# Performance work log

Hardware: AMD Instinct MI355X
Metric: run time of the kernel (lower is better)

## Reference

```python
import jax, jax.numpy as jnp
import numpy as np

T = 5          # Newton-Schulz iterations
EPS = 1e-05


def reference(X):
    # X: (B, C, L); training-mode IterNorm whitening with num_groups=1
    B, C, L = X.shape
    x = jnp.transpose(X, (1, 0, 2)).reshape(C, -1)        # (d, m)
    d, m = x.shape
    mean = jnp.mean(x, axis=-1, keepdims=True)
    xc = x - mean                                         # (d, m)
    I = jnp.eye(d, dtype=X.dtype)
    Sigma = I * EPS + (xc @ xc.T) * (1.0 / m)             # (d, d)
    rTr = 1.0 / jnp.trace(Sigma)                          # scalar
    Sigma_N = Sigma * rTr
    P = I
    for _ in range(T):
        P = 1.5 * P - 0.5 * (P @ P @ P) @ Sigma_N
    wm = P * jnp.sqrt(rTr)                                # whitening matrix
    xn = wm @ xc                                          # (d, m)
    Xn = jnp.transpose(xn.reshape(C, B, L), (1, 0, 2))
    return Xn


def setup_inputs() -> dict:
    key = jax.random.key(0)
    X = jax.random.normal(key, (32, 64, 8192), dtype=jnp.float32)
    return {"X": X}
```

## Files before the change

kernel.cpp:

```cpp
#include <hip/hip_runtime.h>
#include <math.h>

#define L_DIM   8192
#define NCH     64
#define M_TOT_F 262144.0f
#define EPS_F   1e-5f

typedef float f32x4 __attribute__((ext_vector_type(4)));
typedef short bf16x8 __attribute__((ext_vector_type(8)));

union U8 { unsigned u[4]; bf16x8 v; };

__device__ __forceinline__ void cvt2(float f0, float f1, unsigned& h, unsigned& l) {
    unsigned u0 = __float_as_uint(f0), u1 = __float_as_uint(f1);
    h = (u0 >> 16) | (u1 & 0xFFFF0000u);
    float r0 = f0 - __uint_as_float(u0 & 0xFFFF0000u);
    float r1 = f1 - __uint_as_float(u1 & 0xFFFF0000u);
    l = (__float_as_uint(r0) >> 16) | (__float_as_uint(r1) & 0xFFFF0000u);
}

__device__ __forceinline__ void cvt8(const float* p, bf16x8& hi, bf16x8& lo) {
    float4 f0 = *(const float4*)p;
    float4 f1 = *(const float4*)(p + 4);
    U8 H, L;
    cvt2(f0.x, f0.y, H.u[0], L.u[0]);
    cvt2(f0.z, f0.w, H.u[1], L.u[1]);
    cvt2(f1.x, f1.y, H.u[2], L.u[2]);
    cvt2(f1.z, f1.w, H.u[3], L.u[3]);
    hi = H.v; lo = L.v;
}

__device__ __forceinline__ f32x4 mfma16(bf16x8 a, bf16x8 b, f32x4 c) {
    return __builtin_amdgcn_mfma_f32_16x16x32_bf16(a, b, c, 0, 0, 0);
}

__device__ __forceinline__ f32x4 fzero() {
    f32x4 z; z[0] = 0.f; z[1] = 0.f; z[2] = 0.f; z[3] = 0.f; return z;
}

#define GTPB 8
__global__ __launch_bounds__(256) void gram_kernel(const float* __restrict__ X,
                                                   float* __restrict__ P) {
    __shared__ __align__(16) unsigned short hplane[64 * 72];
    __shared__ __align__(16) unsigned short lplane[64 * 72];
    const int tid  = threadIdx.x;
    const int w    = tid >> 6;
    const int lane = tid & 63;
    const int m    = lane & 15;
    const int q    = lane >> 4;
    const int lrow = tid >> 2;
    const int lq16 = (tid & 3) << 4;

    f32x4 acc1[4], acc2[4];
#pragma unroll
    for (int nb = 0; nb < 4; ++nb) { acc1[nb] = fzero(); acc2[nb] = fzero(); }
    float sacc = 0.f;

    const int tile0 = blockIdx.x * GTPB;
    float4 v[4];
    {
        int t = tile0;
        const float* src = X + ((size_t)((t >> 7) * NCH + lrow)) * L_DIM + ((t & 127) << 6) + lq16;
#pragma unroll
        for (int i = 0; i < 4; ++i) v[i] = ((const float4*)src)[i];
    }

    for (int t = 0; t < GTPB; ++t) {
#pragma unroll
        for (int i = 0; i < 4; ++i) sacc += v[i].x + v[i].y + v[i].z + v[i].w;
        __syncthreads();
#pragma unroll
        for (int i = 0; i < 4; ++i) {
            unsigned h0, l0, h1, l1;
            cvt2(v[i].x, v[i].y, h0, l0);
            cvt2(v[i].z, v[i].w, h1, l1);
            uint2 hh; hh.x = h0; hh.y = h1;
            uint2 ll; ll.x = l0; ll.y = l1;
            *(uint2*)&hplane[lrow * 72 + lq16 + 4 * i] = hh;
            *(uint2*)&lplane[lrow * 72 + lq16 + 4 * i] = ll;
        }
        __syncthreads();
        if (t + 1 < GTPB) {
            int tn = tile0 + t + 1;
            const float* src = X + ((size_t)((tn >> 7) * NCH + lrow)) * L_DIM + ((tn & 127) << 6) + lq16;
#pragma unroll
            for (int i = 0; i < 4; ++i) v[i] = ((const float4*)src)[i];
        }
#pragma unroll
        for (int k0 = 0; k0 < 64; k0 += 32) {
            bf16x8 a = *(const bf16x8*)&hplane[(16 * w + m) * 72 + k0 + 8 * q];
#pragma unroll
            for (int nb = 0; nb < 4; ++nb) {
                bf16x8 bh = *(const bf16x8*)&hplane[(16 * nb + m) * 72 + k0 + 8 * q];
                bf16x8 bl = *(const bf16x8*)&lplane[(16 * nb + m) * 72 + k0 + 8 * q];
                acc1[nb] = mfma16(a, bh, acc1[nb]);
                acc2[nb] = mfma16(a, bl, acc2[nb]);
            }
        }
    }

    float* base = P + (size_t)blockIdx.x * 8256;
#pragma unroll
    for (int nb = 0; nb < 4; ++nb)
#pragma unroll
        for (int r = 0; r < 4; ++r) {
            int grow = 16 * w + 4 * q + r;
            int gcol = 16 * nb + m;
            base[grow * 64 + gcol]        = acc1[nb][r];
            base[4096 + grow * 64 + gcol] = acc2[nb][r];
        }
    sacc += __shfl_xor(sacc, 1);
    sacc += __shfl_xor(sacc, 2);
    if ((tid & 3) == 0) base[8192 + lrow] = sacc;
}

__global__ __launch_bounds__(256) void reduce_kernel(const float* __restrict__ P,
                                                     float* __restrict__ ws) {
    const int tid = threadIdx.x;
    const int w = tid >> 6, lane = tid & 63;
    const int e0 = blockIdx.x * 64;
    float a = 0.f;
#pragma unroll 8
    for (int i = 0; i < 128; ++i)
        a += P[(size_t)(w * 128 + i) * 8256 + e0 + lane];
    __shared__ float red[4][64];
    red[w][lane] = a;
    __syncthreads();
    if (w == 0)
        ws[e0 + lane] = red[0][lane] + red[1][lane] + red[2][lane] + red[3][lane];
}

__device__ __forceinline__ void mm_sym(float* __restrict__ D, const float* __restrict__ A,
                                       const float* __restrict__ B, int w, int m, int q) {
    f32x4 acc[4];
#pragma unroll
    for (int nb = 0; nb < 4; ++nb) acc[nb] = fzero();
#pragma unroll
    for (int k0 = 0; k0 < 64; k0 += 32) {
        bf16x8 ah, al;
        cvt8(&A[(16 * w + m) * 68 + k0 + 8 * q], ah, al);
#pragma unroll
        for (int nb = 0; nb < 4; ++nb) {
            bf16x8 bh, bl;
            cvt8(&B[(16 * nb + m) * 68 + k0 + 8 * q], bh, bl);
            acc[nb] = mfma16(ah, bh, acc[nb]);
            acc[nb] = mfma16(ah, bl, acc[nb]);
            acc[nb] = mfma16(al, bh, acc[nb]);
        }
    }
#pragma unroll
    for (int nb = 0; nb < 4; ++nb)
#pragma unroll
        for (int r = 0; r < 4; ++r)
            D[(16 * w + 4 * q + r) * 68 + 16 * nb + m] = acc[nb][r];
}

__global__ __launch_bounds__(256) void ns_kernel(float* __restrict__ ws) {
    __shared__ __align__(16) float S[64 * 68];
    __shared__ __align__(16) float Pm[64 * 68];
    __shared__ __align__(16) float T1[64 * 68];
    __shared__ __align__(16) float T2[64 * 68];
    __shared__ float mu[64];
    __shared__ float scal[2];

    const int tid = threadIdx.x;
    const int w = tid >> 6, lane = tid & 63;
    const int m = lane & 15, q = lane >> 4;
    const float inv_m = 1.0f / M_TOT_F;

    if (tid < 64) mu[tid] = ws[8192 + tid] * inv_m;
    __syncthreads();

    for (int e = tid; e < 4096; e += 256) {
        int i = e >> 6, j = e & 63;
        float g = (ws[e] + ws[4096 + e] + ws[4096 + (j << 6) + i]) * inv_m;
        S[i * 68 + j]  = g - mu[i] * mu[j] + ((i == j) ? EPS_F : 0.f);
        Pm[i * 68 + j] = (i == j) ? 1.f : 0.f;
    }
    __syncthreads();

    if (tid < 64) {
        float v = S[tid * 68 + tid];
#pragma unroll
        for (int off = 32; off >= 1; off >>= 1) v += __shfl_xor(v, off);
        if (tid == 0) { scal[0] = 1.0f / v; scal[1] = sqrtf(1.0f / v); }
    }
    __syncthreads();
    const float rTr = scal[0];
    for (int e = tid; e < 4096; e += 256) S[(e >> 6) * 68 + (e & 63)] *= rTr;
    __syncthreads();

    for (int it = 0; it < 5; ++it) {
        mm_sym(T1, Pm, Pm, w, m, q);
        __syncthreads();
        mm_sym(T2, T1, Pm, w, m, q);
        __syncthreads();
        f32x4 acc[4];
#pragma unroll
        for (int nb = 0; nb < 4; ++nb) acc[nb] = fzero();
#pragma unroll
        for (int k0 = 0; k0 < 64; k0 += 32) {
            bf16x8 ah, al;
            cvt8(&T2[(16 * w + m) * 68 + k0 + 8 * q], ah, al);
#pragma unroll
            for (int nb = 0; nb < 4; ++nb) {
                bf16x8 bh, bl;
                cvt8(&S[(16 * nb + m) * 68 + k0 + 8 * q], bh, bl);
                acc[nb] = mfma16(ah, bh, acc[nb]);
                acc[nb] = mfma16(ah, bl, acc[nb]);
                acc[nb] = mfma16(al, bh, acc[nb]);
            }
        }
#pragma unroll
        for (int nb = 0; nb < 4; ++nb)
#pragma unroll
            for (int r = 0; r < 4; ++r) {
                int idx = (16 * w + 4 * q + r) * 68 + 16 * nb + m;
                Pm[idx] = 1.5f * Pm[idx] - 0.5f * acc[nb][r];
            }
        __syncthreads();
    }

    const float s = scal[1];
    unsigned short* hp = (unsigned short*)ws;
    unsigned short* lp = hp + 4096;
    for (int e = tid; e < 4096; e += 256) {
        int i = e >> 6, j = e & 63;
        float v = Pm[i * 68 + j] * s;
        unsigned u = __float_as_uint(v);
        hp[e] = (unsigned short)(u >> 16);
        float r = v - __uint_as_float(u & 0xFFFF0000u);
        lp[e] = (unsigned short)(__float_as_uint(r) >> 16);
    }
    if (tid < 64) {
        float a = 0.f;
#pragma unroll 8
        for (int k = 0; k < 64; ++k) a += Pm[tid * 68 + k] * mu[k];
        ws[8256 + tid] = -a * s;
    }
}

#define ATPB 4
__global__ __launch_bounds__(256) void apply_kernel(const float* __restrict__ X,
                                                    float* __restrict__ Y,
                                                    const float* __restrict__ ws) {
    __shared__ __align__(16) unsigned short hplane[4096];
    __shared__ __align__(16) unsigned short lplane[4096];
    const int tid  = threadIdx.x;
    const int w    = tid >> 6;
    const int lane = tid & 63;
    const int m    = lane & 15;
    const int q    = lane >> 4;
    const int cp   = tid & 31;
    const int lg   = tid >> 5;

    const unsigned short* hp = (const unsigned short*)ws;
    const unsigned short* lp = hp + 4096;
    bf16x8 Ah[2], Al[2];
#pragma unroll
    for (int kk = 0; kk < 2; ++kk) {
        Ah[kk] = *(const bf16x8*)&hp[(16 * w + m) * 64 + 32 * kk + 8 * q];
        Al[kk] = *(const bf16x8*)&lp[(16 * w + m) * 64 + 32 * kk + 8 * q];
    }
    const float4 bias4 = *(const float4*)&ws[8256 + 16 * w + 4 * q];

    unsigned* hw = (unsigned*)hplane;
    unsigned* lw = (unsigned*)lplane;

    float4 va[2], vb[2];
    {
        int tile = blockIdx.x * ATPB;
        const float* xb = X + (size_t)(tile >> 7) * (NCH * L_DIM) + ((tile & 127) << 6)
                          + (size_t)(2 * cp) * L_DIM + 4 * lg;
#pragma unroll
        for (int s = 0; s < 2; ++s) {
            va[s] = *(const float4*)(xb + 32 * s);
            vb[s] = *(const float4*)(xb + 32 * s + L_DIM);
        }
    }

    for (int t = 0; t < ATPB; ++t) {
        int tile = blockIdx.x * ATPB + t;
        int bidx = tile >> 7;
        int l0   = (tile & 127) << 6;

        __syncthreads();
#pragma unroll
        for (int s = 0; s < 2; ++s) {
            float fa[4], fb[4];
            *(float4*)fa = va[s];
            *(float4*)fb = vb[s];
#pragma unroll
            for (int i = 0; i < 4; ++i) {
                int l = 4 * lg + 32 * s + i;
                unsigned h, lo2;
                cvt2(fa[i], fb[i], h, lo2);
                int widx = l * 32 + (((cp >> 2) ^ (l & 7)) << 2) + (cp & 3);
                hw[widx] = h;
                lw[widx] = lo2;
            }
        }
        __syncthreads();

        if (t + 1 < ATPB) {
            int tn = tile + 1;
            const float* xb = X + (size_t)(tn >> 7) * (NCH * L_DIM) + ((tn & 127) << 6)
                              + (size_t)(2 * cp) * L_DIM + 4 * lg;
#pragma unroll
            for (int s = 0; s < 2; ++s) {
                va[s] = *(const float4*)(xb + 32 * s);
                vb[s] = *(const float4*)(xb + 32 * s + L_DIM);
            }
        }

        f32x4 acc[4];
#pragma unroll
        for (int nb = 0; nb < 4; ++nb) {
            acc[nb][0] = bias4.x; acc[nb][1] = bias4.y;
            acc[nb][2] = bias4.z; acc[nb][3] = bias4.w;
        }
#pragma unroll
        for (int kk = 0; kk < 2; ++kk)
#pragma unroll
            for (int nb = 0; nb < 4; ++nb) {
                int l = 16 * nb + m;
                int saddr = l * 64 + ((((4 * kk + q) ^ (l & 7))) << 3);
                bf16x8 bh = *(const bf16x8*)&hplane[saddr];
                bf16x8 bl = *(const bf16x8*)&lplane[saddr];
                acc[nb] = mfma16(Ah[kk], bh, acc[nb]);
                acc[nb] = mfma16(Ah[kk], bl, acc[nb]);
                acc[nb] = mfma16(Al[kk], bh, acc[nb]);
            }

#pragma unroll
        for (int nb = 0; nb < 4; ++nb)
#pragma unroll
            for (int rr = 0; rr < 4; ++rr)
                Y[((size_t)bidx * NCH + 16 * w + 4 * q + rr) * L_DIM + l0 + 16 * nb + m] = acc[nb][rr];
    }
}

extern "C" void kernel_launch(void* const* d_in, const int* in_sizes, int n_in,
                              void* d_out, int out_size, void* d_ws, size_t ws_size,
                              hipStream_t stream) {
    const float* X = (const float*)d_in[0];
    float* Y  = (float*)d_out;
    float* ws = (float*)d_ws;
    float* scratch = (float*)d_out;

    hipLaunchKernelGGL(gram_kernel,   dim3(512),  dim3(256), 0, stream, X, scratch);
    hipLaunchKernelGGL(reduce_kernel, dim3(129),  dim3(256), 0, stream, scratch, ws);
    hipLaunchKernelGGL(ns_kernel,     dim3(1),    dim3(256), 0, stream, ws);
    hipLaunchKernelGGL(apply_kernel,  dim3(1024), dim3(256), 0, stream, X, Y, ws);
}
```

Before: 157.2 us.

## Parallelize Newton-Schulz over 16 waves with presplit bf16 planes; transpose apply MFMA

The single-block Newton-Schulz kernel now runs 1024 threads. Each of 16 waves computes one 16x16 output tile, and matrices are stored as pre-split bf16 hi/lo planes so the per-load fp32-to-bf16 conversion is gone. The apply kernel swaps MFMA operands: the whitening matrix is held in registers for all four output blocks and X is read from LDS once per k-step. Outputs are written as float4 stores along L instead of scalar stores. This shortens the serial NS latency and widens the output stores, at the cost of more registers in apply and a larger LDS footprint in NS.

```diff
diff --git a/kernel.cpp b/kernel.cpp
--- a/kernel.cpp
+++ b/kernel.cpp
@@ -17,17 +17,6 @@
     float r0 = f0 - __uint_as_float(u0 & 0xFFFF0000u);
     float r1 = f1 - __uint_as_float(u1 & 0xFFFF0000u);
     l = (__float_as_uint(r0) >> 16) | (__float_as_uint(r1) & 0xFFFF0000u);
-}
-
-__device__ __forceinline__ void cvt8(const float* p, bf16x8& hi, bf16x8& lo) {
-    float4 f0 = *(const float4*)p;
-    float4 f1 = *(const float4*)(p + 4);
-    U8 H, L;
-    cvt2(f0.x, f0.y, H.u[0], L.u[0]);
-    cvt2(f0.z, f0.w, H.u[1], L.u[1]);
-    cvt2(f1.x, f1.y, H.u[2], L.u[2]);
-    cvt2(f1.z, f1.w, H.u[3], L.u[3]);
-    hi = H.v; lo = L.v;
 }
 
 __device__ __forceinline__ f32x4 mfma16(bf16x8 a, bf16x8 b, f32x4 c) {
@@ -130,103 +119,115 @@
         ws[e0 + lane] = red[0][lane] + red[1][lane] + red[2][lane] + red[3][lane];
 }
 
-__device__ __forceinline__ void mm_sym(float* __restrict__ D, const float* __restrict__ A,
-                                       const float* __restrict__ B, int w, int m, int q) {
-    f32x4 acc[4];
-#pragma unroll
-    for (int nb = 0; nb < 4; ++nb) acc[nb] = fzero();
+__device__ __forceinline__ void ns_mm(unsigned short* __restrict__ Dh, unsigned short* __restrict__ Dl,
+                                      const unsigned short* __restrict__ Ah, const unsigned short* __restrict__ Al,
+                                      const unsigned short* __restrict__ Bh, const unsigned short* __restrict__ Bl,
+                                      int s, int g, int m, int q) {
+    f32x4 acc = fzero();
 #pragma unroll
     for (int k0 = 0; k0 < 64; k0 += 32) {
-        bf16x8 ah, al;
-        cvt8(&A[(16 * w + m) * 68 + k0 + 8 * q], ah, al);
-#pragma unroll
-        for (int nb = 0; nb < 4; ++nb) {
-            bf16x8 bh, bl;
-            cvt8(&B[(16 * nb + m) * 68 + k0 + 8 * q], bh, bl);
-            acc[nb] = mfma16(ah, bh, acc[nb]);
-            acc[nb] = mfma16(ah, bl, acc[nb]);
-            acc[nb] = mfma16(al, bh, acc[nb]);
-        }
-    }
-#pragma unroll
-    for (int nb = 0; nb < 4; ++nb)
-#pragma unroll
-        for (int r = 0; r < 4; ++r)
-            D[(16 * w + 4 * q + r) * 68 + 16 * nb + m] = acc[nb][r];
-}
-
-__global__ __launch_bounds__(256) void ns_kernel(float* __restrict__ ws) {
-    __shared__ __align__(16) float S[64 * 68];
+        bf16x8 ah = *(const bf16x8*)&Ah[(16 * s + m) * 72 + k0 + 8 * q];
+        bf16x8 al = *(const bf16x8*)&Al[(16 * s + m) * 72 + k0 + 8 * q];
+        bf16x8 bh = *(const bf16x8*)&Bh[(16 * g + m) * 72 + k0 + 8 * q];
+        bf16x8 bl = *(const bf16x8*)&Bl[(16 * g + m) * 72 + k0 + 8 * q];
+        acc = mfma16(ah, bh, acc);
+        acc = mfma16(ah, bl, acc);
+        acc = mfma16(al, bh, acc);
+    }
+#pragma unroll
+    for (int r = 0; r < 4; ++r) {
+        int row = 16 * s + 4 * q + r, col = 16 * g + m;
+        float v = acc[r];
+        unsigned u = __float_as_uint(v);
+        Dh[row * 72 + col] = (unsigned short)(u >> 16);
+        float res = v - __uint_as_float(u & 0xFFFF0000u);
+        Dl[row * 72 + col] = (unsigned short)(__float_as_uint(res) >> 16);
+    }
+}
+
+__global__ __launch_bounds__(1024) void ns_kernel(float* __restrict__ ws) {
     __shared__ __align__(16) float Pm[64 * 68];
-    __shared__ __align__(16) float T1[64 * 68];
-    __shared__ __align__(16) float T2[64 * 68];
+    __shared__ __align__(16) unsigned short Sh[64 * 72],  Sl[64 * 72];
+    __shared__ __align__(16) unsigned short Ph[64 * 72],  Plo[64 * 72];
+    __shared__ __align__(16) unsigned short T1h[64 * 72], T1l[64 * 72];
+    __shared__ __align__(16) unsigned short T2h[64 * 72], T2l[64 * 72];
     __shared__ float mu[64];
     __shared__ float scal[2];
 
     const int tid = threadIdx.x;
-    const int w = tid >> 6, lane = tid & 63;
+    const int w16 = tid >> 6;
+    const int s = w16 >> 2, g = w16 & 3;
+    const int lane = tid & 63;
     const int m = lane & 15, q = lane >> 4;
     const float inv_m = 1.0f / M_TOT_F;
 
     if (tid < 64) mu[tid] = ws[8192 + tid] * inv_m;
     __syncthreads();
 
-    for (int e = tid; e < 4096; e += 256) {
+    for (int e = tid; e < 4096; e += 1024) {
         int i = e >> 6, j = e & 63;
-        float g = (ws[e] + ws[4096 + e] + ws[4096 + (j << 6) + i]) * inv_m;
-        S[i * 68 + j]  = g - mu[i] * mu[j] + ((i == j) ? EPS_F : 0.f);
-        Pm[i * 68 + j] = (i == j) ? 1.f : 0.f;
+        float gv = (ws[e] + ws[4096 + e] + ws[4096 + (j << 6) + i]) * inv_m;
+        Pm[i * 68 + j] = gv - mu[i] * mu[j] + ((i == j) ? EPS_F : 0.f);
     }
     __syncthreads();
 
     if (tid < 64) {
-        float v = S[tid * 68 + tid];
+        float v = Pm[tid * 68 + tid];
 #pragma unroll
         for (int off = 32; off >= 1; off >>= 1) v += __shfl_xor(v, off);
         if (tid == 0) { scal[0] = 1.0f / v; scal[1] = sqrtf(1.0f / v); }
     }
     __syncthreads();
     const float rTr = scal[0];
-    for (int e = tid; e < 4096; e += 256) S[(e >> 6) * 68 + (e & 63)] *= rTr;
+
+    for (int e = tid; e < 4096; e += 1024) {
+        int i = e >> 6, j = e & 63;
+        float v = Pm[i * 68 + j] * rTr;
+        unsigned u = __float_as_uint(v);
+        Sh[i * 72 + j] = (unsigned short)(u >> 16);
+        float res = v - __uint_as_float(u & 0xFFFF0000u);
+        Sl[i * 72 + j] = (unsigned short)(__float_as_uint(res) >> 16);
+        Pm[i * 68 + j] = (i == j) ? 1.f : 0.f;
+        Ph[i * 72 + j] = (i == j) ? (unsigned short)0x3F80 : (unsigned short)0;
+        Plo[i * 72 + j] = 0;
+    }
     __syncthreads();
 
     for (int it = 0; it < 5; ++it) {
-        mm_sym(T1, Pm, Pm, w, m, q);
-        __syncthreads();
-        mm_sym(T2, T1, Pm, w, m, q);
-        __syncthreads();
-        f32x4 acc[4];
-#pragma unroll
-        for (int nb = 0; nb < 4; ++nb) acc[nb] = fzero();
+        ns_mm(T1h, T1l, Ph, Plo, Ph, Plo, s, g, m, q);
+        __syncthreads();
+        ns_mm(T2h, T2l, T1h, T1l, Ph, Plo, s, g, m, q);
+        __syncthreads();
+        f32x4 acc = fzero();
 #pragma unroll
         for (int k0 = 0; k0 < 64; k0 += 32) {
-            bf16x8 ah, al;
-            cvt8(&T2[(16 * w + m) * 68 + k0 + 8 * q], ah, al);
-#pragma unroll
-            for (int nb = 0; nb < 4; ++nb) {
-                bf16x8 bh, bl;
-                cvt8(&S[(16 * nb + m) * 68 + k0 + 8 * q], bh, bl);
-                acc[nb] = mfma16(ah, bh, acc[nb]);
-                acc[nb] = mfma16(ah, bl, acc[nb]);
-                acc[nb] = mfma16(al, bh, acc[nb]);
-            }
-        }
-#pragma unroll
-        for (int nb = 0; nb < 4; ++nb)
-#pragma unroll
-            for (int r = 0; r < 4; ++r) {
-                int idx = (16 * w + 4 * q + r) * 68 + 16 * nb + m;
-                Pm[idx] = 1.5f * Pm[idx] - 0.5f * acc[nb][r];
-            }
-        __syncthreads();
-    }
-
-    const float s = scal[1];
+            bf16x8 ah = *(const bf16x8*)&T2h[(16 * s + m) * 72 + k0 + 8 * q];
+            bf16x8 al = *(const bf16x8*)&T2l[(16 * s + m) * 72 + k0 + 8 * q];
+            bf16x8 bh = *(const bf16x8*)&Sh[(16 * g + m) * 72 + k0 + 8 * q];
+            bf16x8 bl = *(const bf16x8*)&Sl[(16 * g + m) * 72 + k0 + 8 * q];
+            acc = mfma16(ah, bh, acc);
+            acc = mfma16(ah, bl, acc);
+            acc = mfma16(al, bh, acc);
+        }
+#pragma unroll
+        for (int r = 0; r < 4; ++r) {
+            int row = 16 * s + 4 * q + r, col = 16 * g + m;
+            float pv = 1.5f * Pm[row * 68 + col] - 0.5f * acc[r];
+            Pm[row * 68 + col] = pv;
+            unsigned u = __float_as_uint(pv);
+            Ph[row * 72 + col] = (unsigned short)(u >> 16);
+            float res = pv - __uint_as_float(u & 0xFFFF0000u);
+            Plo[row * 72 + col] = (unsigned short)(__float_as_uint(res) >> 16);
+        }
+        __syncthreads();
+    }
+
+    const float sc = scal[1];
     unsigned short* hp = (unsigned short*)ws;
     unsigned short* lp = hp + 4096;
-    for (int e = tid; e < 4096; e += 256) {
+    for (int e = tid; e < 4096; e += 1024) {
         int i = e >> 6, j = e & 63;
-        float v = Pm[i * 68 + j] * s;
+        float v = Pm[i * 68 + j] * sc;
         unsigned u = __float_as_uint(v);
         hp[e] = (unsigned short)(u >> 16);
         float r = v - __uint_as_float(u & 0xFFFF0000u);
@@ -236,7 +237,7 @@
         float a = 0.f;
 #pragma unroll 8
         for (int k = 0; k < 64; ++k) a += Pm[tid * 68 + k] * mu[k];
-        ws[8256 + tid] = -a * s;
+        ws[8256 + tid] = -a * sc;
     }
 }
 
@@ -256,13 +257,17 @@
 
     const unsigned short* hp = (const unsigned short*)ws;
     const unsigned short* lp = hp + 4096;
-    bf16x8 Ah[2], Al[2];
-#pragma unroll
-    for (int kk = 0; kk < 2; ++kk) {
-        Ah[kk] = *(const bf16x8*)&hp[(16 * w + m) * 64 + 32 * kk + 8 * q];
-        Al[kk] = *(const bf16x8*)&lp[(16 * w + m) * 64 + 32 * kk + 8 * q];
-    }
-    const float4 bias4 = *(const float4*)&ws[8256 + 16 * w + 4 * q];
+    bf16x8 Wh[4][2], Wl[4][2];
+#pragma unroll
+    for (int nb = 0; nb < 4; ++nb)
+#pragma unroll
+        for (int kk = 0; kk < 2; ++kk) {
+            Wh[nb][kk] = *(const bf16x8*)&hp[(16 * nb + m) * 64 + 32 * kk + 8 * q];
+            Wl[nb][kk] = *(const bf16x8*)&lp[(16 * nb + m) * 64 + 32 * kk + 8 * q];
+        }
+    float biasv[4];
+#pragma unroll
+    for (int nb = 0; nb < 4; ++nb) biasv[nb] = ws[8256 + 16 * nb + m];
 
     unsigned* hw = (unsigned*)hplane;
     unsigned* lw = (unsigned*)lplane;
@@ -273,9 +278,9 @@
         const float* xb = X + (size_t)(tile >> 7) * (NCH * L_DIM) + ((tile & 127) << 6)
                           + (size_t)(2 * cp) * L_DIM + 4 * lg;
 #pragma unroll
-        for (int s = 0; s < 2; ++s) {
-            va[s] = *(const float4*)(xb + 32 * s);
-            vb[s] = *(const float4*)(xb + 32 * s + L_DIM);
+        for (int ss = 0; ss < 2; ++ss) {
+            va[ss] = *(const float4*)(xb + 32 * ss);
+            vb[ss] = *(const float4*)(xb + 32 * ss + L_DIM);
         }
     }
 
@@ -286,13 +291,13 @@
 
         __syncthreads();
 #pragma unroll
-        for (int s = 0; s < 2; ++s) {
+        for (int ss = 0; ss < 2; ++ss) {
             float fa[4], fb[4];
-            *(float4*)fa = va[s];
-            *(float4*)fb = vb[s];
+            *(float4*)fa = va[ss];
+            *(float4*)fb = vb[ss];
 #pragma unroll
             for (int i = 0; i < 4; ++i) {
-                int l = 4 * lg + 32 * s + i;
+                int l = 4 * lg + 32 * ss + i;
                 unsigned h, lo2;
                 cvt2(fa[i], fb[i], h, lo2);
                 int widx = l * 32 + (((cp >> 2) ^ (l & 7)) << 2) + (cp & 3);
@@ -307,36 +312,38 @@
             const float* xb = X + (size_t)(tn >> 7) * (NCH * L_DIM) + ((tn & 127) << 6)
                               + (size_t)(2 * cp) * L_DIM + 4 * lg;
 #pragma unroll
-            for (int s = 0; s < 2; ++s) {
-                va[s] = *(const float4*)(xb + 32 * s);
-                vb[s] = *(const float4*)(xb + 32 * s + L_DIM);
+            for (int ss = 0; ss < 2; ++ss) {
+                va[ss] = *(const float4*)(xb + 32 * ss);
+                vb[ss] = *(const float4*)(xb + 32 * ss + L_DIM);
             }
         }
 
         f32x4 acc[4];
 #pragma unroll
         for (int nb = 0; nb < 4; ++nb) {
-            acc[nb][0] = bias4.x; acc[nb][1] = bias4.y;
-            acc[nb][2] = bias4.z; acc[nb][3] = bias4.w;
-        }
-#pragma unroll
-        for (int kk = 0; kk < 2; ++kk)
+            acc[nb][0] = biasv[nb]; acc[nb][1] = biasv[nb];
+            acc[nb][2] = biasv[nb]; acc[nb][3] = biasv[nb];
+        }
+#pragma unroll
+        for (int kk = 0; kk < 2; ++kk) {
+            const int l = 16 * w + m;
+            const int saddr = l * 64 + ((((4 * kk + q) ^ (l & 7))) << 3);
+            bf16x8 xh = *(const bf16x8*)&hplane[saddr];
+            bf16x8 xl = *(const bf16x8*)&lplane[saddr];
 #pragma unroll
             for (int nb = 0; nb < 4; ++nb) {
-                int l = 16 * nb + m;
-                int saddr = l * 64 + ((((4 * kk + q) ^ (l & 7))) << 3);
-                bf16x8 bh = *(const bf16x8*)&hplane[saddr];
-                bf16x8 bl = *(const bf16x8*)&lplane[saddr];
-                acc[nb] = mfma16(Ah[kk], bh, acc[nb]);
-                acc[nb] = mfma16(Ah[kk], bl, acc[nb]);
-                acc[nb] = mfma16(Al[kk], bh, acc[nb]);
+                acc[nb] = mfma16(xh, Wh[nb][kk], acc[nb]);
+                acc[nb] = mfma16(xh, Wl[nb][kk], acc[nb]);
+                acc[nb] = mfma16(xl, Wh[nb][kk], acc[nb]);
             }
-
-#pragma unroll
-        for (int nb = 0; nb < 4; ++nb)
-#pragma unroll
-            for (int rr = 0; rr < 4; ++rr)
-                Y[((size_t)bidx * NCH + 16 * w + 4 * q + rr) * L_DIM + l0 + 16 * nb + m] = acc[nb][rr];
+        }
+
+#pragma unroll
+        for (int nb = 0; nb < 4; ++nb) {
+            float4 o;
+            o.x = acc[nb][0]; o.y = acc[nb][1]; o.z = acc[nb][2]; o.w = acc[nb][3];
+            *(float4*)&Y[((size_t)bidx * NCH + 16 * nb + m) * L_DIM + l0 + 16 * w + 4 * q] = o;
+        }
     }
 }
 
@@ -350,6 +357,6 @@
 
     hipLaunchKernelGGL(gram_kernel,   dim3(512),  dim3(256), 0, stream, X, scratch);
     hipLaunchKernelGGL(reduce_kernel, dim3(129),  dim3(256), 0, stream, scratch, ws);
-    hipLaunchKernelGGL(ns_kernel,     dim3(1),    dim3(256), 0, stream, ws);
+    hipLaunchKernelGGL(ns_kernel,     dim3(1),    dim3(1024), 0, stream, ws);
     hipLaunchKernelGGL(apply_kernel,  dim3(1024), dim3(256), 0, stream, X, Y, ws);
 }
```

Measured after the change: 160.2 us. No clear change (+1.9%).
